# Kernel optimization log

Measured on AMD Instinct MI355X. Metric: run time of the kernel, lower is better.

## Reference

```python
import jax, jax.numpy as jnp
import numpy as np

POOLED_H = 7
POOLED_W = 7
SAMPLING_RATIO = 2


def setup_inputs() -> dict:
    key = jax.random.key(0)
    k1, k2, k3, k4 = jax.random.split(key, 4)
    B, C, H, W = 2, 256, 192, 192
    N = 1024
    stride = 16
    img_h, img_w = H * stride, W * stride
    feature = jax.random.normal(k1, (B, C, H, W), dtype=jnp.float32)
    # well-formed rois: (batch_idx, x1, y1, x2, y2) in image coordinates
    bidx = jax.random.randint(k2, (N, 1), 0, B).astype(jnp.float32)
    p1 = jax.random.uniform(k3, (N, 2), minval=0.0, maxval=0.7)
    wh = jax.random.uniform(k4, (N, 2), minval=0.02, maxval=0.3)
    x1y1 = p1 * jnp.array([img_w, img_h], jnp.float32)
    x2y2 = jnp.minimum(x1y1 + wh * jnp.array([img_w, img_h], jnp.float32),
                       jnp.array([img_w - 1.0, img_h - 1.0], jnp.float32))
    rois = jnp.concatenate([bidx, x1y1[:, :1], x1y1[:, 1:], x2y2[:, :1], x2y2[:, 1:]], axis=1)
    return {"rois": rois, "feature": feature, "stride": stride}


def _roi_align(feature, rois, pooled_h, pooled_w, spatial_scale, ratio):
    B, C, H, W = feature.shape
    N = rois.shape[0]
    b = rois[:, 0].astype(jnp.int32)                     # [N]
    x1 = rois[:, 1] * spatial_scale
    y1 = rois[:, 2] * spatial_scale
    x2 = rois[:, 3] * spatial_scale
    y2 = rois[:, 4] * spatial_scale
    roi_w = jnp.maximum(x2 - x1, 1.0)                    # classic (non-aligned) RoIAlign
    roi_h = jnp.maximum(y2 - y1, 1.0)
    bin_w = roi_w / pooled_w
    bin_h = roi_h / pooled_h

    Sy, Sx = pooled_h * ratio, pooled_w * ratio
    iy = (jnp.arange(Sy, dtype=feature.dtype) + 0.5) / ratio  # in units of bin_h
    ix = (jnp.arange(Sx, dtype=feature.dtype) + 0.5) / ratio
    y = y1[:, None] + iy[None, :] * bin_h[:, None]       # [N, Sy]
    x = x1[:, None] + ix[None, :] * bin_w[:, None]       # [N, Sx]

    def interp_axis(c, size):
        valid = (c > -1.0) & (c < size)
        cc = jnp.clip(c, 0.0, size - 1)
        lo = jnp.floor(cc).astype(jnp.int32)
        lo = jnp.minimum(lo, size - 1)
        hi = jnp.minimum(lo + 1, size - 1)
        frac = cc - lo.astype(c.dtype)
        return valid, lo, hi, frac

    vy, y0, y1i, fy = interp_axis(y, H)
    vx, x0, x1i, fx = interp_axis(x, W)

    hy, ly = (1.0 - fy), fy                              # [N, Sy]
    hx, lx = (1.0 - fx), fx                              # [N, Sx]

    bI = b[:, None, None]

    def gather(yi, xi):
        # -> [N, Sy, Sx, C]
        return feature[bI, :, yi[:, :, None], xi[:, None, :]]

    val = (hy[:, :, None] * hx[:, None, :])[..., None] * gather(y0, x0) \
        + (hy[:, :, None] * lx[:, None, :])[..., None] * gather(y0, x1i) \
        + (ly[:, :, None] * hx[:, None, :])[..., None] * gather(y1i, x0) \
        + (ly[:, :, None] * lx[:, None, :])[..., None] * gather(y1i, x1i)
    val = val * (vy[:, :, None] & vx[:, None, :])[..., None].astype(val.dtype)

    # average sampling grid within each bin
    out = val.reshape(N, pooled_h, ratio, pooled_w, ratio, C).mean(axis=(2, 4))
    return out.transpose(0, 3, 1, 2)                     # [N, C, pooled_h, pooled_w]


def reference(rois, feature, stride):
    rois = rois[:, :5].astype(feature.dtype)
    spatial_scale = 1.0 / stride
    return _roi_align(feature, rois, POOLED_H, POOLED_W, spatial_scale, SAMPLING_RATIO)
```

## Files before the change

kernel.cpp:

```cpp
#include <hip/hip_runtime.h>
#include <hip/hip_fp16.h>

#define POOLED 7
#define RATIO 2

constexpr int C_ = 256;
constexpr int H_ = 192;
constexpr int W_ = 192;
constexpr int P_ = H_ * W_;
constexpr int PP2 = POOLED * POOLED;

constexpr int TC = 32;
constexpr int TP = 128;
constexpr int TPAD = TP + 1;

__global__ __launch_bounds__(256)
void nchw_to_nhwc_h(const float* __restrict__ in, __half* __restrict__ outT) {
    __shared__ float tile[TC][TPAD];
    const int b  = blockIdx.z;
    const int p0 = blockIdx.x * TP;
    const int c0 = blockIdx.y * TC;
    const float* src = in   + (size_t)b * C_ * P_;
    __half*      dst = outT + (size_t)b * P_ * C_;

    const int t = threadIdx.x;

    #pragma unroll
    for (int k = 0; k < 4; ++k) {
        const int q  = t + 256 * k;
        const int c  = q >> 5;
        const int pv = q & 31;
        const float4 v = *(const float4*)&src[(size_t)(c0 + c) * P_ + p0 + 4 * pv];
        tile[c][4 * pv + 0] = v.x;
        tile[c][4 * pv + 1] = v.y;
        tile[c][4 * pv + 2] = v.z;
        tile[c][4 * pv + 3] = v.w;
    }
    __syncthreads();

    #pragma unroll
    for (int k = 0; k < 2; ++k) {
        const int q  = t + 256 * k;
        const int p  = q >> 2;
        const int c8 = (q & 3) * 8;
        union { __half h[8]; float4 f; } u;
        #pragma unroll
        for (int i = 0; i < 8; ++i) u.h[i] = __float2half(tile[c8 + i][p]);
        *(float4*)&dst[(size_t)(p0 + p) * C_ + c0 + c8] = u.f;
    }
}

constexpr int CB  = 64;
constexpr int BPR = C_ / CB;
constexpr int BST = CB + 2;

__global__ __launch_bounds__(256, 8)
void roi_align_nhwc_h(const float* __restrict__ rois,
                      const __half* __restrict__ featT,
                      const int* __restrict__ stride_ptr,
                      float* __restrict__ out, int N) {
    __shared__ __half lds_out[PP2 * BST];
    __shared__ int4 coord[28];

    const int blk  = blockIdx.x;
    const int n    = blk >> 2;
    const int cq   = blk & 3;
    const int t    = threadIdx.x;
    const int lane = t & 63;
    const int wave = t >> 6;

    const float scale = 1.0f / (float)stride_ptr[0];
    const float* r = rois + (size_t)n * 5;
    const int   b   = (int)r[0];
    const float rx1 = r[1] * scale;
    const float ry1 = r[2] * scale;
    const float rx2 = r[3] * scale;
    const float ry2 = r[4] * scale;
    const float bin_w = fmaxf(rx2 - rx1, 1.0f) * (1.0f / (float)POOLED);
    const float bin_h = fmaxf(ry2 - ry1, 1.0f) * (1.0f / (float)POOLED);

    if (t < 28) {
        const bool  isY   = t < 14;
        const int   s     = isY ? t : t - 14;
        const float start = isY ? ry1 : rx1;
        const float bsz   = isY ? bin_h : bin_w;
        const int   size  = isY ? H_ : W_;
        const float cc0   = start + ((float)s + 0.5f) * 0.5f * bsz;
        const bool  valid = (cc0 > -1.0f) && (cc0 < (float)size);
        float cc = fminf(fmaxf(cc0, 0.0f), (float)(size - 1));
        int lo = (int)floorf(cc);
        if (lo > size - 1) lo = size - 1;
        const int hi = min(lo + 1, size - 1);
        const float frac = (cc - (float)lo) * 0.5f;
        int4 e;
        e.x = isY ? lo * W_ : lo;
        e.y = isY ? hi * W_ : hi;
        e.z = __float_as_int(frac);
        e.w = valid ? 1 : 0;
        coord[t] = e;
    }
    __syncthreads();

    const uint4* fbase = (const uint4*)featT + (size_t)b * P_ * (C_ / 8);
    const int cl4   = cq * (CB / 8) + (lane & 7);
    const int g     = lane >> 3;
    const int sxsel = g >> 2;
    const int ysel  = (g >> 1) & 1;
    const int xsel  = g & 1;

    auto mkbin = [&](int bin, int& o0, int& o1, __half2& w0, __half2& w1) {
        const int ph = bin / POOLED;
        const int pw = bin - ph * POOLED;
        const int4  cx  = coord[14 + 2 * pw + sxsel];
        const float fx  = __int_as_float(cx.z);
        const float wx  = xsel ? fx : 0.5f - fx;
        const int   col = xsel ? cx.y : cx.x;

        const int4  cy0  = coord[2 * ph + 0];
        const float fy0  = __int_as_float(cy0.z);
        float wf0 = (ysel ? fy0 : 0.5f - fy0) * wx;
        if (!(cy0.w & cx.w)) wf0 = 0.0f;
        o0 = ((ysel ? cy0.y : cy0.x) + col) * (C_ / 8) + cl4;
        w0 = __float2half2_rn(wf0);

        const int4  cy1  = coord[2 * ph + 1];
        const float fy1  = __int_as_float(cy1.z);
        float wf1 = (ysel ? fy1 : 0.5f - fy1) * wx;
        if (!(cy1.w & cx.w)) wf1 = 0.0f;
        o1 = ((ysel ? cy1.y : cy1.x) + col) * (C_ / 8) + cl4;
        w1 = __float2half2_rn(wf1);
    };

    auto compute_store = [&](int bin, const uint4& A, const uint4& B,
                             __half2 W0, __half2 W1) {
        __half2 a0 = __hmul2(W0, *(const __half2*)&A.x);
        __half2 a1 = __hmul2(W0, *(const __half2*)&A.y);
        __half2 a2 = __hmul2(W0, *(const __half2*)&A.z);
        __half2 a3 = __hmul2(W0, *(const __half2*)&A.w);
        a0 = __hfma2(W1, *(const __half2*)&B.x, a0);
        a1 = __hfma2(W1, *(const __half2*)&B.y, a1);
        a2 = __hfma2(W1, *(const __half2*)&B.z, a2);
        a3 = __hfma2(W1, *(const __half2*)&B.w, a3);

        union HI { __half2 h; int i; };
        #pragma unroll
        for (int d = 8; d <= 32; d <<= 1) {
            HI u0, u1, u2, u3, s0, s1, s2, s3;
            u0.h = a0; u1.h = a1; u2.h = a2; u3.h = a3;
            s0.i = __shfl_xor(u0.i, d, 64);
            s1.i = __shfl_xor(u1.i, d, 64);
            s2.i = __shfl_xor(u2.i, d, 64);
            s3.i = __shfl_xor(u3.i, d, 64);
            a0 = __hadd2(a0, s0.h);
            a1 = __hadd2(a1, s1.h);
            a2 = __hadd2(a2, s2.h);
            a3 = __hadd2(a3, s3.h);
        }
        if (lane < 8) {
            __half2* dst = (__half2*)&lds_out[bin * BST + lane * 8];
            dst[0] = a0; dst[1] = a1; dst[2] = a2; dst[3] = a3;
        }
    };

    const int bin_lo = (wave * PP2) >> 2;
    const int bin_hi = ((wave + 1) * PP2) >> 2;

    int o0, o1; __half2 w0, w1;
    mkbin(bin_lo, o0, o1, w0, w1);
    uint4 vA = fbase[(unsigned)o0];
    uint4 vB = fbase[(unsigned)o1];

    for (int bin = bin_lo; bin < bin_hi - 1; ++bin) {
        int no0, no1; __half2 nw0, nw1;
        mkbin(bin + 1, no0, no1, nw0, nw1);
        const uint4 pA = fbase[(unsigned)no0];
        const uint4 pB = fbase[(unsigned)no1];
        compute_store(bin, vA, vB, w0, w1);
        vA = pA; vB = pB; w0 = nw0; w1 = nw1;
    }
    compute_store(bin_hi - 1, vA, vB, w0, w1);

    __syncthreads();

    float4* o4 = (float4*)(out + (size_t)n * (C_ * PP2) + (size_t)cq * (CB * PP2));
    for (int i = t; i < (CB * PP2) / 4; i += 256) {
        const int l0 = i * 4;
        float4 v;
        #pragma unroll
        for (int j = 0; j < 4; ++j) {
            const int l  = l0 + j;
            const int c  = l / PP2;
            const int bn = l - c * PP2;
            ((float*)&v)[j] = __half2float(lds_out[bn * BST + c]);
        }
        o4[i] = v;
    }
}

__global__ __launch_bounds__(256)
void roi_align_kernel(const float* __restrict__ rois,
                      const float* __restrict__ feat,
                      const int* __restrict__ stride_ptr,
                      int B, int C, int H, int W, int N,
                      float* __restrict__ out) {
    const int total = N * C * POOLED * POOLED;
    int idx = blockIdx.x * blockDim.x + threadIdx.x;
    if (idx >= total) return;

    const float scale = 1.0f / (float)stride_ptr[0];

    int pw = idx % POOLED;
    int ph = (idx / POOLED) % POOLED;
    int c  = (idx / (POOLED * POOLED)) % C;
    int n  = idx / (POOLED * POOLED * C);

    const float* r = rois + (size_t)n * 5;
    int b = (int)r[0];
    float x1 = r[1] * scale;
    float y1 = r[2] * scale;
    float x2 = r[3] * scale;
    float y2 = r[4] * scale;
    float bin_w = fmaxf(x2 - x1, 1.0f) / (float)POOLED;
    float bin_h = fmaxf(y2 - y1, 1.0f) / (float)POOLED;

    const float* plane = feat + ((size_t)b * C + c) * (size_t)(H * W);

    float acc = 0.0f;
    #pragma unroll
    for (int sy = 0; sy < RATIO; ++sy) {
        float iy = ((float)(ph * RATIO + sy) + 0.5f) / (float)RATIO;
        float yy = y1 + iy * bin_h;
        bool vy = (yy > -1.0f) && (yy < (float)H);
        float cy = fminf(fmaxf(yy, 0.0f), (float)(H - 1));
        int y0 = (int)floorf(cy);
        if (y0 > H - 1) y0 = H - 1;
        int y1i = min(y0 + 1, H - 1);
        float fy = cy - (float)y0;
        float hy = 1.0f - fy;

        #pragma unroll
        for (int sx = 0; sx < RATIO; ++sx) {
            float ix = ((float)(pw * RATIO + sx) + 0.5f) / (float)RATIO;
            float xx = x1 + ix * bin_w;
            bool vx = (xx > -1.0f) && (xx < (float)W);
            if (!(vy && vx)) continue;
            float cx = fminf(fmaxf(xx, 0.0f), (float)(W - 1));
            int x0 = (int)floorf(cx);
            if (x0 > W - 1) x0 = W - 1;
            int x1i = min(x0 + 1, W - 1);
            float fx = cx - (float)x0;
            float hx = 1.0f - fx;

            float v00 = plane[y0  * W + x0 ];
            float v01 = plane[y0  * W + x1i];
            float v10 = plane[y1i * W + x0 ];
            float v11 = plane[y1i * W + x1i];

            acc += hy * hx * v00 + hy * fx * v01 + fy * hx * v10 + fy * fx * v11;
        }
    }

    out[idx] = acc * 0.25f;
}

extern "C" void kernel_launch(void* const* d_in, const int* in_sizes, int n_in,
                              void* d_out, int out_size, void* d_ws, size_t ws_size,
                              hipStream_t stream) {
    const float* rois = (const float*)d_in[0];
    const float* feat = (const float*)d_in[1];
    const int* stride_ptr = (const int*)d_in[2];

    const int N = in_sizes[0] / 5;
    const int B = in_sizes[1] / (C_ * P_);
    float* out = (float*)d_out;

    const size_t need = (size_t)B * P_ * C_ * sizeof(__half);
    if (ws_size >= need) {
        __half* featT = (__half*)d_ws;
        dim3 tgrid(P_ / TP, C_ / TC, B);
        nchw_to_nhwc_h<<<tgrid, 256, 0, stream>>>(feat, featT);

        roi_align_nhwc_h<<<N * BPR, 256, 0, stream>>>(rois, featT, stride_ptr, out, N);
    } else {
        const int total = N * C_ * POOLED * POOLED;
        const int block = 256;
        const int grid = (total + block - 1) / block;
        roi_align_kernel<<<grid, block, 0, stream>>>(rois, feat, stride_ptr,
                                                     B, C_, H_, W_, N, out);
    }
}
```

Measured before the change: 164.7 us.

## Partition RoIs by batch index and schedule blocks per batch-channel class

Adds a single-block kernel that sorts RoI indices into per-batch lists using wave ballots and LDS atomics. The RoIAlign kernel becomes persistent: each of its 8 block classes (batch × channel quarter) walks one batch's list with a grid stride. The aim is to keep concurrently running blocks on the same batch image and channel slice, so the transposed feature map is reused better in cache. The cost is an extra serial launch, a dependency on counts read from global memory, a loop with an extra sync per RoI, and an assumption of only two batches (b & 1).

```diff
diff --git a/kernel.cpp b/kernel.cpp
--- a/kernel.cpp
+++ b/kernel.cpp
@@ -50,6 +50,32 @@
     }
 }
 
+__global__ __launch_bounds__(1024)
+void roi_partition(const float* __restrict__ rois, int N,
+                   int* __restrict__ lists,
+                   int* __restrict__ counts) {
+    __shared__ int cnt[2];
+    const int t    = threadIdx.x;
+    const int lane = t & 63;
+    if (t < 2) cnt[t] = 0;
+    __syncthreads();
+
+    for (int i = t; i < N; i += 1024) {
+        const int b = ((int)rois[(size_t)i * 5]) & 1;
+        const unsigned long long m0 = __ballot(b == 0);
+        const unsigned long long m1 = __ballot(b == 1);
+        const unsigned long long mine = b ? m1 : m0;
+        const int first = __ffsll((long long)mine) - 1;
+        const int rank  = __popcll(mine & ((1ull << lane) - 1ull));
+        int base = 0;
+        if (lane == first) base = atomicAdd(&cnt[b], (int)__popcll(mine));
+        base = __shfl(base, first, 64);
+        lists[b * N + base + rank] = i;
+    }
+    __syncthreads();
+    if (t < 2) counts[t] = cnt[t];
+}
+
 constexpr int CB  = 64;
 constexpr int BPR = C_ / CB;
 constexpr int BST = CB + 2;
@@ -58,142 +84,153 @@
 void roi_align_nhwc_h(const float* __restrict__ rois,
                       const __half* __restrict__ featT,
                       const int* __restrict__ stride_ptr,
+                      const int* __restrict__ lists,
+                      const int* __restrict__ counts,
                       float* __restrict__ out, int N) {
     __shared__ __half lds_out[PP2 * BST];
     __shared__ int4 coord[28];
 
-    const int blk  = blockIdx.x;
-    const int n    = blk >> 2;
-    const int cq   = blk & 3;
     const int t    = threadIdx.x;
     const int lane = t & 63;
     const int wave = t >> 6;
 
+    const int cls  = blockIdx.x & 7;
+    const int bsel = cls >> 2;
+    const int cq   = cls & 3;
+    const int nb   = counts[bsel];
+    const int slots = (int)(gridDim.x >> 3);
+
     const float scale = 1.0f / (float)stride_ptr[0];
-    const float* r = rois + (size_t)n * 5;
-    const int   b   = (int)r[0];
-    const float rx1 = r[1] * scale;
-    const float ry1 = r[2] * scale;
-    const float rx2 = r[3] * scale;
-    const float ry2 = r[4] * scale;
-    const float bin_w = fmaxf(rx2 - rx1, 1.0f) * (1.0f / (float)POOLED);
-    const float bin_h = fmaxf(ry2 - ry1, 1.0f) * (1.0f / (float)POOLED);
-
-    if (t < 28) {
-        const bool  isY   = t < 14;
-        const int   s     = isY ? t : t - 14;
-        const float start = isY ? ry1 : rx1;
-        const float bsz   = isY ? bin_h : bin_w;
-        const int   size  = isY ? H_ : W_;
-        const float cc0   = start + ((float)s + 0.5f) * 0.5f * bsz;
-        const bool  valid = (cc0 > -1.0f) && (cc0 < (float)size);
-        float cc = fminf(fmaxf(cc0, 0.0f), (float)(size - 1));
-        int lo = (int)floorf(cc);
-        if (lo > size - 1) lo = size - 1;
-        const int hi = min(lo + 1, size - 1);
-        const float frac = (cc - (float)lo) * 0.5f;
-        int4 e;
-        e.x = isY ? lo * W_ : lo;
-        e.y = isY ? hi * W_ : hi;
-        e.z = __float_as_int(frac);
-        e.w = valid ? 1 : 0;
-        coord[t] = e;
-    }
-    __syncthreads();
-
-    const uint4* fbase = (const uint4*)featT + (size_t)b * P_ * (C_ / 8);
+
     const int cl4   = cq * (CB / 8) + (lane & 7);
     const int g     = lane >> 3;
     const int sxsel = g >> 2;
     const int ysel  = (g >> 1) & 1;
     const int xsel  = g & 1;
 
-    auto mkbin = [&](int bin, int& o0, int& o1, __half2& w0, __half2& w1) {
-        const int ph = bin / POOLED;
-        const int pw = bin - ph * POOLED;
-        const int4  cx  = coord[14 + 2 * pw + sxsel];
-        const float fx  = __int_as_float(cx.z);
-        const float wx  = xsel ? fx : 0.5f - fx;
-        const int   col = xsel ? cx.y : cx.x;
-
-        const int4  cy0  = coord[2 * ph + 0];
-        const float fy0  = __int_as_float(cy0.z);
-        float wf0 = (ysel ? fy0 : 0.5f - fy0) * wx;
-        if (!(cy0.w & cx.w)) wf0 = 0.0f;
-        o0 = ((ysel ? cy0.y : cy0.x) + col) * (C_ / 8) + cl4;
-        w0 = __float2half2_rn(wf0);
-
-        const int4  cy1  = coord[2 * ph + 1];
-        const float fy1  = __int_as_float(cy1.z);
-        float wf1 = (ysel ? fy1 : 0.5f - fy1) * wx;
-        if (!(cy1.w & cx.w)) wf1 = 0.0f;
-        o1 = ((ysel ? cy1.y : cy1.x) + col) * (C_ / 8) + cl4;
-        w1 = __float2half2_rn(wf1);
-    };
-
-    auto compute_store = [&](int bin, const uint4& A, const uint4& B,
-                             __half2 W0, __half2 W1) {
-        __half2 a0 = __hmul2(W0, *(const __half2*)&A.x);
-        __half2 a1 = __hmul2(W0, *(const __half2*)&A.y);
-        __half2 a2 = __hmul2(W0, *(const __half2*)&A.z);
-        __half2 a3 = __hmul2(W0, *(const __half2*)&A.w);
-        a0 = __hfma2(W1, *(const __half2*)&B.x, a0);
-        a1 = __hfma2(W1, *(const __half2*)&B.y, a1);
-        a2 = __hfma2(W1, *(const __half2*)&B.z, a2);
-        a3 = __hfma2(W1, *(const __half2*)&B.w, a3);
-
-        union HI { __half2 h; int i; };
-        #pragma unroll
-        for (int d = 8; d <= 32; d <<= 1) {
-            HI u0, u1, u2, u3, s0, s1, s2, s3;
-            u0.h = a0; u1.h = a1; u2.h = a2; u3.h = a3;
-            s0.i = __shfl_xor(u0.i, d, 64);
-            s1.i = __shfl_xor(u1.i, d, 64);
-            s2.i = __shfl_xor(u2.i, d, 64);
-            s3.i = __shfl_xor(u3.i, d, 64);
-            a0 = __hadd2(a0, s0.h);
-            a1 = __hadd2(a1, s1.h);
-            a2 = __hadd2(a2, s2.h);
-            a3 = __hadd2(a3, s3.h);
+    for (int j = (int)(blockIdx.x >> 3); j < nb; j += slots) {
+        const int n = lists[bsel * N + j];
+
+        const float* r = rois + (size_t)n * 5;
+        const int   b   = (int)r[0];
+        const float rx1 = r[1] * scale;
+        const float ry1 = r[2] * scale;
+        const float rx2 = r[3] * scale;
+        const float ry2 = r[4] * scale;
+        const float bin_w = fmaxf(rx2 - rx1, 1.0f) * (1.0f / (float)POOLED);
+        const float bin_h = fmaxf(ry2 - ry1, 1.0f) * (1.0f / (float)POOLED);
+
+        if (t < 28) {
+            const bool  isY   = t < 14;
+            const int   s     = isY ? t : t - 14;
+            const float start = isY ? ry1 : rx1;
+            const float bsz   = isY ? bin_h : bin_w;
+            const int   size  = isY ? H_ : W_;
+            const float cc0   = start + ((float)s + 0.5f) * 0.5f * bsz;
+            const bool  valid = (cc0 > -1.0f) && (cc0 < (float)size);
+            float cc = fminf(fmaxf(cc0, 0.0f), (float)(size - 1));
+            int lo = (int)floorf(cc);
+            if (lo > size - 1) lo = size - 1;
+            const int hi = min(lo + 1, size - 1);
+            const float frac = (cc - (float)lo) * 0.5f;
+            int4 e;
+            e.x = isY ? lo * W_ : lo;
+            e.y = isY ? hi * W_ : hi;
+            e.z = __float_as_int(frac);
+            e.w = valid ? 1 : 0;
+            coord[t] = e;
         }
-        if (lane < 8) {
-            __half2* dst = (__half2*)&lds_out[bin * BST + lane * 8];
-            dst[0] = a0; dst[1] = a1; dst[2] = a2; dst[3] = a3;
+        __syncthreads();
+
+        const uint4* fbase = (const uint4*)featT + (size_t)b * P_ * (C_ / 8);
+
+        auto mkbin = [&](int bin, int& o0, int& o1, __half2& w0, __half2& w1) {
+            const int ph = bin / POOLED;
+            const int pw = bin - ph * POOLED;
+            const int4  cx  = coord[14 + 2 * pw + sxsel];
+            const float fx  = __int_as_float(cx.z);
+            const float wx  = xsel ? fx : 0.5f - fx;
+            const int   col = xsel ? cx.y : cx.x;
+
+            const int4  cy0  = coord[2 * ph + 0];
+            const float fy0  = __int_as_float(cy0.z);
+            float wf0 = (ysel ? fy0 : 0.5f - fy0) * wx;
+            if (!(cy0.w & cx.w)) wf0 = 0.0f;
+            o0 = ((ysel ? cy0.y : cy0.x) + col) * (C_ / 8) + cl4;
+            w0 = __float2half2_rn(wf0);
+
+            const int4  cy1  = coord[2 * ph + 1];
+            const float fy1  = __int_as_float(cy1.z);
+            float wf1 = (ysel ? fy1 : 0.5f - fy1) * wx;
+            if (!(cy1.w & cx.w)) wf1 = 0.0f;
+            o1 = ((ysel ? cy1.y : cy1.x) + col) * (C_ / 8) + cl4;
+            w1 = __float2half2_rn(wf1);
+        };
+
+        auto compute_store = [&](int bin, const uint4& A, const uint4& B,
+                                 __half2 W0, __half2 W1) {
+            __half2 a0 = __hmul2(W0, *(const __half2*)&A.x);
+            __half2 a1 = __hmul2(W0, *(const __half2*)&A.y);
+            __half2 a2 = __hmul2(W0, *(const __half2*)&A.z);
+            __half2 a3 = __hmul2(W0, *(const __half2*)&A.w);
+            a0 = __hfma2(W1, *(const __half2*)&B.x, a0);
+            a1 = __hfma2(W1, *(const __half2*)&B.y, a1);
+            a2 = __hfma2(W1, *(const __half2*)&B.z, a2);
+            a3 = __hfma2(W1, *(const __half2*)&B.w, a3);
+
+            union HI { __half2 h; int i; };
+            #pragma unroll
+            for (int d = 8; d <= 32; d <<= 1) {
+                HI u0, u1, u2, u3, s0, s1, s2, s3;
+                u0.h = a0; u1.h = a1; u2.h = a2; u3.h = a3;
+                s0.i = __shfl_xor(u0.i, d, 64);
+                s1.i = __shfl_xor(u1.i, d, 64);
+                s2.i = __shfl_xor(u2.i, d, 64);
+                s3.i = __shfl_xor(u3.i, d, 64);
+                a0 = __hadd2(a0, s0.h);
+                a1 = __hadd2(a1, s1.h);
+                a2 = __hadd2(a2, s2.h);
+                a3 = __hadd2(a3, s3.h);
+            }
+            if (lane < 8) {
+                __half2* dst = (__half2*)&lds_out[bin * BST + lane * 8];
+                dst[0] = a0; dst[1] = a1; dst[2] = a2; dst[3] = a3;
+            }
+        };
+
+        const int bin_lo = (wave * PP2) >> 2;
+        const int bin_hi = ((wave + 1) * PP2) >> 2;
+
+        int o0, o1; __half2 w0, w1;
+        mkbin(bin_lo, o0, o1, w0, w1);
+        uint4 vA = fbase[(unsigned)o0];
+        uint4 vB = fbase[(unsigned)o1];
+
+        for (int bin = bin_lo; bin < bin_hi - 1; ++bin) {
+            int no0, no1; __half2 nw0, nw1;
+            mkbin(bin + 1, no0, no1, nw0, nw1);
+            const uint4 pA = fbase[(unsigned)no0];
+            const uint4 pB = fbase[(unsigned)no1];
+            compute_store(bin, vA, vB, w0, w1);
+            vA = pA; vB = pB; w0 = nw0; w1 = nw1;
         }
-    };
-
-    const int bin_lo = (wave * PP2) >> 2;
-    const int bin_hi = ((wave + 1) * PP2) >> 2;
-
-    int o0, o1; __half2 w0, w1;
-    mkbin(bin_lo, o0, o1, w0, w1);
-    uint4 vA = fbase[(unsigned)o0];
-    uint4 vB = fbase[(unsigned)o1];
-
-    for (int bin = bin_lo; bin < bin_hi - 1; ++bin) {
-        int no0, no1; __half2 nw0, nw1;
-        mkbin(bin + 1, no0, no1, nw0, nw1);
-        const uint4 pA = fbase[(unsigned)no0];
-        const uint4 pB = fbase[(unsigned)no1];
-        compute_store(bin, vA, vB, w0, w1);
-        vA = pA; vB = pB; w0 = nw0; w1 = nw1;
-    }
-    compute_store(bin_hi - 1, vA, vB, w0, w1);
-
-    __syncthreads();
-
-    float4* o4 = (float4*)(out + (size_t)n * (C_ * PP2) + (size_t)cq * (CB * PP2));
-    for (int i = t; i < (CB * PP2) / 4; i += 256) {
-        const int l0 = i * 4;
-        float4 v;
-        #pragma unroll
-        for (int j = 0; j < 4; ++j) {
-            const int l  = l0 + j;
-            const int c  = l / PP2;
-            const int bn = l - c * PP2;
-            ((float*)&v)[j] = __half2float(lds_out[bn * BST + c]);
+        compute_store(bin_hi - 1, vA, vB, w0, w1);
+
+        __syncthreads();
+
+        float4* o4 = (float4*)(out + (size_t)n * (C_ * PP2) + (size_t)cq * (CB * PP2));
+        for (int i = t; i < (CB * PP2) / 4; i += 256) {
+            const int l0 = i * 4;
+            float4 v;
+            #pragma unroll
+            for (int jj = 0; jj < 4; ++jj) {
+                const int l  = l0 + jj;
+                const int c  = l / PP2;
+                const int bn = l - c * PP2;
+                ((float*)&v)[jj] = __half2float(lds_out[bn * BST + c]);
+            }
+            o4[i] = v;
         }
-        o4[i] = v;
     }
 }
 
@@ -274,13 +311,23 @@
     const int B = in_sizes[1] / (C_ * P_);
     float* out = (float*)d_out;
 
-    const size_t need = (size_t)B * P_ * C_ * sizeof(__half);
+    const size_t featBytes = (size_t)B * P_ * C_ * sizeof(__half);
+    const size_t featAl    = (featBytes + 255) & ~(size_t)255;
+    const size_t need      = featAl + (size_t)(2 * N + 2) * sizeof(int);
+
     if (ws_size >= need) {
-        __half* featT = (__half*)d_ws;
+        __half* featT  = (__half*)d_ws;
+        int*    lists  = (int*)((char*)d_ws + featAl);
+        int*    counts = lists + 2 * N;
+
         dim3 tgrid(P_ / TP, C_ / TC, B);
         nchw_to_nhwc_h<<<tgrid, 256, 0, stream>>>(feat, featT);
 
-        roi_align_nhwc_h<<<N * BPR, 256, 0, stream>>>(rois, featT, stride_ptr, out, N);
+        roi_partition<<<1, 1024, 0, stream>>>(rois, N, lists, counts);
+
+        const int slots = N < 512 ? (N > 0 ? N : 1) : 512;
+        roi_align_nhwc_h<<<8 * slots, 256, 0, stream>>>(rois, featT, stride_ptr,
+                                                        lists, counts, out, N);
     } else {
         const int total = N * C_ * POOLED * POOLED;
         const int block = 256;
```

After: 168.3 us. 1.02x slower.
